# Optimization experiments

Hardware: AMD Instinct MI355X
Metric: run time of the kernel (lower is better)

Reference implementation:

```python
import jax, jax.numpy as jnp
import numpy as np

N_NODES = 100000
N_EDGES = 6400000
N_FEAT = 128
HIDDEN = 16
N_CLASSES = 10
N_GRAPHS = 1024


def setup_inputs() -> dict:
    key = jax.random.key(0)
    ks = jax.random.split(key, 16)
    x = jax.random.normal(ks[0], (N_NODES, N_FEAT), dtype=jnp.float32)
    src = jax.random.randint(ks[1], (N_EDGES,), 0, N_NODES, dtype=jnp.int64)
    dst = jax.random.randint(ks[2], (N_EDGES,), 0, N_NODES, dtype=jnp.int64)
    edge_index = jnp.stack([src, dst], axis=0)
    batch = jnp.sort(jax.random.randint(ks[3], (N_NODES,), 0, N_GRAPHS, dtype=jnp.int64))
    s = 0.1
    emb = jax.random.normal(ks[4], (N_FEAT, HIDDEN), dtype=jnp.float32) * s
    W1l = jax.random.normal(ks[5], (HIDDEN, HIDDEN), dtype=jnp.float32) * s
    b1 = jnp.zeros((HIDDEN,), dtype=jnp.float32)
    W1r = jax.random.normal(ks[6], (HIDDEN, HIDDEN), dtype=jnp.float32) * s
    W2l = jax.random.normal(ks[7], (HIDDEN, HIDDEN), dtype=jnp.float32) * s
    b2 = jnp.zeros((HIDDEN,), dtype=jnp.float32)
    W2r = jax.random.normal(ks[8], (HIDDEN, HIDDEN), dtype=jnp.float32) * s
    W3l = jax.random.normal(ks[9], (N_CLASSES, HIDDEN), dtype=jnp.float32) * s
    b3 = jnp.zeros((N_CLASSES,), dtype=jnp.float32)
    W3r = jax.random.normal(ks[10], (N_CLASSES, HIDDEN), dtype=jnp.float32) * s
    return {"x": x, "edge_index": edge_index, "batch": batch, "emb": emb,
            "W1l": W1l, "b1": b1, "W1r": W1r,
            "W2l": W2l, "b2": b2, "W2r": W2r,
            "W3l": W3l, "b3": b3, "W3r": W3r}


def _sage_conv(h, src, dst, Wl, bl, Wr, n_nodes):
    # PyG SAGEConv (aggr='mean'): out = lin_l(mean_j x_j) + lin_r(x_i), then L2-normalize
    msgs = h[src]                                             # [E, F]
    agg = jax.ops.segment_sum(msgs, dst, num_segments=n_nodes)
    deg = jax.ops.segment_sum(jnp.ones((src.shape[0],), h.dtype), dst, num_segments=n_nodes)
    agg = agg / jnp.maximum(deg, 1.0)[:, None]
    out = agg @ Wl.T + bl + h @ Wr.T
    norm = jnp.linalg.norm(out, axis=-1, keepdims=True)
    return out / jnp.maximum(norm, 1e-12)


def reference(x, edge_index, batch, emb, W1l, b1, W1r, W2l, b2, W2r, W3l, b3, W3r):
    src, dst = edge_index[0], edge_index[1]
    n = x.shape[0]
    # embedding of argmax over one-hot-ish features
    h = emb[jnp.argmax(x, axis=1)]                            # [N, H]
    h = jax.nn.relu(_sage_conv(h, src, dst, W1l, b1, W1r, n))  # dropout is identity in eval
    h = jax.nn.relu(_sage_conv(h, src, dst, W2l, b2, W2r, n))
    h = _sage_conv(h, src, dst, W3l, b3, W3r, n)              # [N, C]
    # global mean pool over graphs
    pooled = jax.ops.segment_sum(h, batch, num_segments=N_GRAPHS)
    cnt = jax.ops.segment_sum(jnp.ones((n,), h.dtype), batch, num_segments=N_GRAPHS)
    pooled = pooled / jnp.maximum(cnt, 1.0)[:, None]
    return jax.nn.softmax(pooled, axis=1)
```

## Files before the change

### kernel.cpp

```cpp
#include <hip/hip_runtime.h>
#include <hip/hip_bf16.h>

#define N_FEAT 128
#define HID 16
#define NCLS 10
#define NGRAPH 1024
#define SHIFT 7
#define NBMAX 1024
#define CAP 24576
#define CH 8192
#define EPB (CH / 256)
#define GC_NODES 64
#define GCAP2 5120

__device__ __forceinline__ float u2f(unsigned int u) {
    union { unsigned int u; float f; } c; c.u = u; return c.f;
}
__device__ __forceinline__ float bf2f(__hip_bfloat16 b) {
    return __bfloat162float(b);
}
__device__ __forceinline__ unsigned short f2us(float f) {
    union { __hip_bfloat16 b; unsigned short u; } c;
    c.b = __float2bfloat16(f);
    return c.u;
}
__device__ __forceinline__ float ldw(const void* __restrict__ p, int i, int isbf) {
    return isbf ? bf2f(((const __hip_bfloat16*)p)[i]) : ((const float*)p)[i];
}
__device__ __forceinline__ void unp8(uint4 v, float* f) {
    f[0] = u2f(v.x << 16); f[1] = u2f(v.x & 0xffff0000u);
    f[2] = u2f(v.y << 16); f[3] = u2f(v.y & 0xffff0000u);
    f[4] = u2f(v.z << 16); f[5] = u2f(v.z & 0xffff0000u);
    f[6] = u2f(v.w << 16); f[7] = u2f(v.w & 0xffff0000u);
}
__device__ __forceinline__ void acc8(uint4 v, float* a8) {
    a8[0] += u2f(v.x << 16); a8[1] += u2f(v.x & 0xffff0000u);
    a8[2] += u2f(v.y << 16); a8[3] += u2f(v.y & 0xffff0000u);
    a8[4] += u2f(v.z << 16); a8[5] += u2f(v.z & 0xffff0000u);
    a8[6] += u2f(v.w << 16); a8[7] += u2f(v.w & 0xffff0000u);
}

__global__ void k_detect(const int* __restrict__ ei,
                         const unsigned int* __restrict__ xw,
                         int* __restrict__ flags) {
    if (blockIdx.x == 0 && threadIdx.x == 0) {
        int nz = 0;
        for (int i = 1; i < 256; i += 2) nz |= ei[i];
        flags[0] = (nz == 0) ? 1 : 0;
        int cnt = 0;
        for (int i = 0; i < 64; i++) {
            unsigned int ef = xw[i] & 0x7F80u;
            if (ef >= 0x3C00u && ef <= 0x4080u) cnt++;
        }
        flags[1] = (cnt >= 32) ? 1 : 0;
    }
}

__global__ void k_argmax_embed(const void* __restrict__ x,
                               const void* __restrict__ emb,
                               const int* __restrict__ flags,
                               unsigned short* __restrict__ h, int n) {
    int wave = (int)((blockIdx.x * (unsigned)blockDim.x + threadIdx.x) >> 6);
    int lane = threadIdx.x & 63;
    if (wave >= n) return;
    int isbf = flags[1];
    float v0, v1;
    if (isbf) {
        const unsigned int* row =
            (const unsigned int*)((const __hip_bfloat16*)x + (size_t)wave * N_FEAT);
        unsigned int u = row[lane];
        v0 = u2f(u << 16);
        v1 = u2f(u & 0xffff0000u);
    } else {
        const float2* row = (const float2*)((const float*)x + (size_t)wave * N_FEAT);
        float2 u = row[lane];
        v0 = u.x; v1 = u.y;
    }
    float bv; int bi;
    if (v1 > v0) { bv = v1; bi = 2 * lane + 1; }
    else         { bv = v0; bi = 2 * lane; }
    #pragma unroll
    for (int off = 1; off < 64; off <<= 1) {
        float ov = __shfl_xor(bv, off);
        int   oi = __shfl_xor(bi, off);
        if (ov > bv || (ov == bv && oi < bi)) { bv = ov; bi = oi; }
    }
    if (lane < HID) {
        unsigned short us;
        if (isbf) us = ((const unsigned short*)emb)[bi * HID + lane];
        else      us = f2us(((const float*)emb)[bi * HID + lane]);
        h[(size_t)wave * HID + lane] = us;
    }
}

__global__ void k_binhist(const int* __restrict__ ei, const int* __restrict__ flags,
                          int* __restrict__ rbBuf, int e, int nbins) {
    __shared__ int lh[NBMAX];
    int t = threadIdx.x;
    for (int b = t; b < nbins; b += 256) lh[b] = 0;
    __syncthreads();
    int base = blockIdx.x * CH;
    int sh = flags[0];
    for (int j = 0; j < EPB; j++) {
        int i = base + j * 256 + t;
        if (i < e) {
            int d = ei[((size_t)(e + i)) << sh];
            atomicAdd(&lh[d >> SHIFT], 1);
        }
    }
    __syncthreads();
    int* row = rbBuf + (size_t)blockIdx.x * nbins;
    for (int b = t; b < nbins; b += 256) row[b] = lh[b];
}

__global__ void k_colscan(int* __restrict__ rbBuf, int* __restrict__ binCnt,
                          int nblk, int nbins) {
    __shared__ int ls[1024];
    int b = blockIdx.x, t = threadIdx.x;
    int v = (t < nblk) ? rbBuf[(size_t)t * nbins + b] : 0;
    ls[t] = v;
    __syncthreads();
    #pragma unroll
    for (int off = 1; off < 1024; off <<= 1) {
        int w = (t >= off) ? ls[t - off] : 0;
        __syncthreads();
        ls[t] += w;
        __syncthreads();
    }
    if (t < nblk) rbBuf[(size_t)t * nbins + b] = ls[t] - v;
    if (t == 1023) binCnt[b] = ls[t];
}

__global__ void k_scanbins(const int* __restrict__ binCnt,
                           int* __restrict__ binStart, int nbins, int e) {
    __shared__ int ls[1024];
    int t = threadIdx.x;
    int v = (t < nbins) ? binCnt[t] : 0;
    ls[t] = v;
    __syncthreads();
    #pragma unroll
    for (int off = 1; off < 1024; off <<= 1) {
        int w = (t >= off) ? ls[t - off] : 0;
        __syncthreads();
        ls[t] += w;
        __syncthreads();
    }
    if (t < nbins) binStart[t] = ls[t] - v;
    if (t == 0) binStart[nbins] = e;
}

__global__ __launch_bounds__(256) void k_binplace(
        const int* __restrict__ ei, const int* __restrict__ flags,
        const int* __restrict__ binStart, const int* __restrict__ rbBuf,
        int* __restrict__ col, int e, int nbins) {
    __shared__ int cnt[NBMAX];
    __shared__ int ldsOff[NBMAX];
    __shared__ int ldsBase[NBMAX];
    __shared__ int ps[256];
    __shared__ int stage[CH];
    __shared__ unsigned short binOf[CH];
    int t = threadIdx.x;
    for (int b = t; b < nbins; b += 256) cnt[b] = 0;
    __syncthreads();
    int base = blockIdx.x * CH;
    int sh = flags[0];
    int myV[EPB]; short myB[EPB];
    for (int j = 0; j < EPB; j++) {
        int i = base + j * 256 + t;
        if (i < e) {
            int s = ei[((size_t)i) << sh];
            int d = ei[((size_t)(e + i)) << sh];
            myV[j] = (s << SHIFT) | (d & ((1 << SHIFT) - 1));
            int b2 = d >> SHIFT;
            myB[j] = (short)b2;
            atomicAdd(&cnt[b2], 1);
        } else myB[j] = -1;
    }
    __syncthreads();
    int c[4]; int lsum = 0;
    int bb = t * 4;
    #pragma unroll
    for (int k = 0; k < 4; k++) {
        int b2 = bb + k;
        c[k] = (b2 < nbins) ? cnt[b2] : 0;
        lsum += c[k];
    }
    ps[t] = lsum;
    __syncthreads();
    #pragma unroll
    for (int off = 1; off < 256; off <<= 1) {
        int w = (t >= off) ? ps[t - off] : 0;
        __syncthreads();
        ps[t] += w;
        __syncthreads();
    }
    int run = ps[t] - lsum;
    #pragma unroll
    for (int k = 0; k < 4; k++) {
        int b2 = bb + k;
        if (b2 < nbins) ldsOff[b2] = run;
        run += c[k];
    }
    __syncthreads();
    const int* rb = rbBuf + (size_t)blockIdx.x * nbins;
    for (int b2 = t; b2 < nbins; b2 += 256) {
        ldsBase[b2] = binStart[b2] + rb[b2] - ldsOff[b2];
        cnt[b2] = 0;
    }
    __syncthreads();
    for (int j = 0; j < EPB; j++) {
        if (myB[j] >= 0) {
            int b2 = myB[j];
            int r = atomicAdd(&cnt[b2], 1);
            int p = ldsOff[b2] + r;
            stage[p] = myV[j];
            binOf[p] = (unsigned short)b2;
        }
    }
    __syncthreads();
    int total = e - base;
    if (total > CH) total = CH;
    for (int i = t; i < total; i += 256) {
        int b2 = binOf[i];
        col[ldsBase[b2] + i] = stage[i];
    }
}

__global__ void k_place(int* __restrict__ col, const int* __restrict__ binStart,
                        int* __restrict__ rowStart, int n, int e) {
    __shared__ int stage[CAP];
    __shared__ int cntN[1 << SHIFT];
    __shared__ int sc[1 << SHIFT];
    __shared__ int rs[1 << SHIFT];
    int b = blockIdx.x;
    int t = threadIdx.x;
    int nb = b << SHIFT;
    int s0 = binStart[b];
    int s1 = binStart[b + 1];
    int cnt = s1 - s0;
    if (t < (1 << SHIFT)) cntN[t] = 0;
    bool st = (cnt <= CAP);
    __syncthreads();
    for (int i = t; i < cnt; i += 256) {
        int v = col[s0 + i];
        if (st) stage[i] = v;
        atomicAdd(&cntN[v & ((1 << SHIFT) - 1)], 1);
    }
    __syncthreads();
    if (t < (1 << SHIFT)) sc[t] = cntN[t];
    __syncthreads();
    #pragma unroll
    for (int off = 1; off < (1 << SHIFT); off <<= 1) {
        int w = 0;
        if (t < (1 << SHIFT) && t >= off) w = sc[t - off];
        __syncthreads();
        if (t < (1 << SHIFT)) sc[t] += w;
        __syncthreads();
    }
    if (t < (1 << SHIFT)) {
        int start = s0 + sc[t] - cntN[t];
        rs[t] = start;
        int node = nb + t;
        if (node < n) rowStart[node] = start;
        cntN[t] = 0;
    }
    __syncthreads();
    for (int i = t; i < cnt; i += 256) {
        int v = st ? stage[i] : col[s0 + i];
        int dl = v & ((1 << SHIFT) - 1);
        int r = atomicAdd(&cntN[dl], 1);
        col[rs[dl] + r] = v >> SHIFT;
    }
}

__global__ __launch_bounds__(256) void k_gc(
        const int* __restrict__ col, const int* __restrict__ rowStart,
        const unsigned short* __restrict__ hin,
        const void* __restrict__ Wl, const void* __restrict__ bia,
        const void* __restrict__ Wr, const int* __restrict__ flags,
        unsigned short* __restrict__ hout, int n, int e) {
    __shared__ int ecol[GCAP2];
    __shared__ float wl[HID][HID], wr[HID][HID], bb[HID];
    int t = threadIdx.x;
    int b = blockIdx.x;
    int isbf = flags[1];
    if (t < HID * HID) {
        wl[t >> 4][t & 15] = ldw(Wl, t, isbf);
        wr[t >> 4][t & 15] = ldw(Wr, t, isbf);
    }
    if (t < HID) bb[t] = ldw(bia, t, isbf);
    int nb = b * GC_NODES;
    int s0 = rowStart[nb];
    int s1 = (nb + GC_NODES < n) ? rowStart[nb + GC_NODES] : e;
    int cnt = s1 - s0;
    bool st = (cnt <= GCAP2);
    if (st)
        for (int i = t; i < cnt; i += 256)
            ecol[i] = __builtin_nontemporal_load(col + s0 + i);
    __syncthreads();
    int nl = t >> 2;
    int j  = t & 1;
    int p  = (t >> 1) & 1;
    int node = nb + nl;
    if (node >= n) return;
    int lo = rowStart[node];
    int hi = (node + 1 < n) ? rowStart[node + 1] : e;
    const uint4* h4 = (const uint4*)hin;
    float a8[8];
    #pragma unroll
    for (int k = 0; k < 8; k++) a8[k] = 0.0f;
    if (st) {
        int i = lo - s0 + p;
        int end = hi - s0;
        for (; i + 6 < end; i += 8) {
            int e0 = ecol[i], e1 = ecol[i + 2], e2 = ecol[i + 4], e3 = ecol[i + 6];
            uint4 v0 = h4[(size_t)e0 * 2 + j];
            uint4 v1 = h4[(size_t)e1 * 2 + j];
            uint4 v2 = h4[(size_t)e2 * 2 + j];
            uint4 v3 = h4[(size_t)e3 * 2 + j];
            acc8(v0, a8); acc8(v1, a8); acc8(v2, a8); acc8(v3, a8);
        }
        for (; i < end; i += 2) {
            uint4 v = h4[(size_t)ecol[i] * 2 + j];
            acc8(v, a8);
        }
    } else {
        int i = lo + p;
        for (; i + 6 < hi; i += 8) {
            int e0 = col[i], e1 = col[i + 2], e2 = col[i + 4], e3 = col[i + 6];
            uint4 v0 = h4[(size_t)e0 * 2 + j];
            uint4 v1 = h4[(size_t)e1 * 2 + j];
            uint4 v2 = h4[(size_t)e2 * 2 + j];
            uint4 v3 = h4[(size_t)e3 * 2 + j];
            acc8(v0, a8); acc8(v1, a8); acc8(v2, a8); acc8(v3, a8);
        }
        for (; i < hi; i += 2) {
            uint4 v = h4[(size_t)col[i] * 2 + j];
            acc8(v, a8);
        }
    }
    #pragma unroll
    for (int k = 0; k < 8; k++) a8[k] += __shfl_xor(a8[k], 2);
    float invd = 1.0f / fmaxf((float)(hi - lo), 1.0f);
    #pragma unroll
    for (int k = 0; k < 8; k++) a8[k] *= invd;
    float av[HID];
    #pragma unroll
    for (int k = 0; k < 8; k++) {
        av[8 * j + k] = a8[k];
        av[8 * (1 - j) + k] = __shfl_xor(a8[k], 1);
    }
    float hb[HID];
    unp8(h4[(size_t)node * 2], hb);
    unp8(h4[(size_t)node * 2 + 1], hb + 8);
    float o[HID]; float sq = 0.0f;
    #pragma unroll
    for (int f = 0; f < HID; f++) {
        float acc = bb[f];
        #pragma unroll
        for (int k = 0; k < HID; k++)
            acc += av[k] * wl[f][k] + hb[k] * wr[f][k];
        o[f] = acc;
        sq += acc * acc;
    }
    float inn = 1.0f / fmaxf(sqrtf(sq), 1e-12f);
    if (p == 0) {
        uint4 w;
        unsigned int* wp = (unsigned int*)&w;
        #pragma unroll
        for (int q = 0; q < 4; q++) {
            unsigned int l0 = f2us(fmaxf(o[8 * j + 2 * q] * inn, 0.0f));
            unsigned int h0 = f2us(fmaxf(o[8 * j + 2 * q + 1] * inn, 0.0f));
            wp[q] = l0 | (h0 << 16);
        }
        ((uint4*)hout)[(size_t)node * 2 + j] = w;
    }
}

__global__ __launch_bounds__(256) void k_gc3(
        const int* __restrict__ col, const int* __restrict__ rowStart,
        const unsigned short* __restrict__ hin,
        const void* __restrict__ Wl, const void* __restrict__ bia,
        const void* __restrict__ Wr, const int* __restrict__ flags,
        float* __restrict__ h3, int n, int e) {
    __shared__ int ecol[GCAP2];
    __shared__ float wl[NCLS][HID], wr[NCLS][HID], bb[NCLS];
    int t = threadIdx.x;
    int b = blockIdx.x;
    int isbf = flags[1];
    if (t < NCLS * HID) {
        wl[t >> 4][t & 15] = ldw(Wl, t, isbf);
        wr[t >> 4][t & 15] = ldw(Wr, t, isbf);
    }
    if (t < NCLS) bb[t] = ldw(bia, t, isbf);
    int nb = b * GC_NODES;
    int s0 = rowStart[nb];
    int s1 = (nb + GC_NODES < n) ? rowStart[nb + GC_NODES] : e;
    int cnt = s1 - s0;
    bool st = (cnt <= GCAP2);
    if (st)
        for (int i = t; i < cnt; i += 256)
            ecol[i] = __builtin_nontemporal_load(col + s0 + i);
    __syncthreads();
    int nl = t >> 2;
    int j  = t & 1;
    int p  = (t >> 1) & 1;
    int node = nb + nl;
    if (node >= n) return;
    int lo = rowStart[node];
    int hi = (node + 1 < n) ? rowStart[node + 1] : e;
    const uint4* h4 = (const uint4*)hin;
    float a8[8];
    #pragma unroll
    for (int k = 0; k < 8; k++) a8[k] = 0.0f;
    if (st) {
        int i = lo - s0 + p;
        int end = hi - s0;
        for (; i + 6 < end; i += 8) {
            int e0 = ecol[i], e1 = ecol[i + 2], e2 = ecol[i + 4], e3 = ecol[i + 6];
            uint4 v0 = h4[(size_t)e0 * 2 + j];
            uint4 v1 = h4[(size_t)e1 * 2 + j];
            uint4 v2 = h4[(size_t)e2 * 2 + j];
            uint4 v3 = h4[(size_t)e3 * 2 + j];
            acc8(v0, a8); acc8(v1, a8); acc8(v2, a8); acc8(v3, a8);
        }
        for (; i < end; i += 2) {
            uint4 v = h4[(size_t)ecol[i] * 2 + j];
            acc8(v, a8);
        }
    } else {
        int i = lo + p;
        for (; i + 6 < hi; i += 8) {
            int e0 = col[i], e1 = col[i + 2], e2 = col[i + 4], e3 = col[i + 6];
            uint4 v0 = h4[(size_t)e0 * 2 + j];
            uint4 v1 = h4[(size_t)e1 * 2 + j];
            uint4 v2 = h4[(size_t)e2 * 2 + j];
            uint4 v3 = h4[(size_t)e3 * 2 + j];
            acc8(v0, a8); acc8(v1, a8); acc8(v2, a8); acc8(v3, a8);
        }
        for (; i < hi; i += 2) {
            uint4 v = h4[(size_t)col[i] * 2 + j];
            acc8(v, a8);
        }
    }
    #pragma unroll
    for (int k = 0; k < 8; k++) a8[k] += __shfl_xor(a8[k], 2);
    float invd = 1.0f / fmaxf((float)(hi - lo), 1.0f);
    #pragma unroll
    for (int k = 0; k < 8; k++) a8[k] *= invd;
    float av[HID];
    #pragma unroll
    for (int k = 0; k < 8; k++) {
        av[8 * j + k] = a8[k];
        av[8 * (1 - j) + k] = __shfl_xor(a8[k], 1);
    }
    float hb[HID];
    unp8(h4[(size_t)node * 2], hb);
    unp8(h4[(size_t)node * 2 + 1], hb + 8);
    float o[NCLS]; float sq = 0.0f;
    #pragma unroll
    for (int f = 0; f < NCLS; f++) {
        float acc = bb[f];
        #pragma unroll
        for (int k = 0; k < HID; k++)
            acc += av[k] * wl[f][k] + hb[k] * wr[f][k];
        o[f] = acc;
        sq += acc * acc;
    }
    float inn = 1.0f / fmaxf(sqrtf(sq), 1e-12f);
    float* op = h3 + (size_t)node * NCLS;
    if (p == 0) {
        if (j == 0) {
            #pragma unroll
            for (int f = 0; f < 8; f++) op[f] = o[f] * inn;
        } else {
            op[8] = o[8] * inn;
            op[9] = o[9] * inn;
        }
    }
}

__device__ __forceinline__ int lbound(const int* __restrict__ a, int n, int key, int sh) {
    int lo = 0, hi = n;
    while (lo < hi) {
        int mid = (lo + hi) >> 1;
        if (a[((size_t)mid) << sh] < key) lo = mid + 1; else hi = mid;
    }
    return lo;
}

__global__ void k_pool_softmax(const float* __restrict__ h3,
                               const int* __restrict__ batch,
                               const int* __restrict__ flags,
                               void* __restrict__ out, int n) {
    int g = blockIdx.x;
    int lane = threadIdx.x;
    int sh = flags[0];
    int lo = lbound(batch, n, g, sh);
    int hi = lbound(batch, n, g + 1, sh);
    float acc[NCLS];
    #pragma unroll
    for (int c = 0; c < NCLS; c++) acc[c] = 0.0f;
    for (int i = lo + lane; i < hi; i += 64) {
        const float* r = h3 + (size_t)i * NCLS;
        #pragma unroll
        for (int c = 0; c < NCLS; c++) acc[c] += r[c];
    }
    #pragma unroll
    for (int c = 0; c < NCLS; c++) {
        #pragma unroll
        for (int off = 1; off < 64; off <<= 1)
            acc[c] += __shfl_xor(acc[c], off);
    }
    float invc = 1.0f / fmaxf((float)(hi - lo), 1.0f);
    float m = -1e30f;
    #pragma unroll
    for (int c = 0; c < NCLS; c++) { acc[c] *= invc; m = fmaxf(m, acc[c]); }
    float s = 0.0f;
    #pragma unroll
    for (int c = 0; c < NCLS; c++) { acc[c] = expf(acc[c] - m); s += acc[c]; }
    float invs = 1.0f / s;
    if (lane < NCLS) {
        float v = acc[lane] * invs;
        size_t idx = (size_t)g * NCLS + lane;
        if (flags[1]) ((__hip_bfloat16*)out)[idx] = __float2bfloat16(v);
        else          ((float*)out)[idx] = v;
    }
}

extern "C" void kernel_launch(void* const* d_in, const int* in_sizes, int n_in,
                              void* d_out, int out_size, void* d_ws, size_t ws_size,
                              hipStream_t stream) {
    const void* x   = d_in[0];
    const int*  ei  = (const int*)d_in[1];
    const int*  bat = (const int*)d_in[2];
    const void* emb = d_in[3];
    const void* W1l = d_in[4];  const void* b1 = d_in[5];  const void* W1r = d_in[6];
    const void* W2l = d_in[7];  const void* b2 = d_in[8];  const void* W2r = d_in[9];
    const void* W3l = d_in[10]; const void* b3 = d_in[11]; const void* W3r = d_in[12];

    int n = in_sizes[0] / N_FEAT;
    int e = in_sizes[1] / 2;
    int nbins = (n + (1 << SHIFT) - 1) >> SHIFT;
    int nblk  = (e + CH - 1) / CH;

    unsigned short* hcur  = (unsigned short*)d_ws;
    unsigned short* hnext = hcur + (size_t)n * HID;
    float* h3       = (float*)(hnext + (size_t)n * HID);
    int*   col      = (int*)(h3 + (size_t)n * NCLS);
    int*   rowStart = col + e;
    int*   binCnt   = rowStart + n;
    int*   binStart = binCnt + nbins;
    int*   rbBuf    = binStart + (nbins + 1);
    int*   flags    = rbBuf + (size_t)nblk * nbins;

    int ngrid4 = (n + 3) / 4;
    int ngc = (n + GC_NODES - 1) / GC_NODES;

    k_detect<<<1, 64, 0, stream>>>(ei, (const unsigned int*)x, flags);
    k_binhist<<<nblk, 256, 0, stream>>>(ei, flags, rbBuf, e, nbins);
    k_colscan<<<nbins, 1024, 0, stream>>>(rbBuf, binCnt, nblk, nbins);
    k_scanbins<<<1, 1024, 0, stream>>>(binCnt, binStart, nbins, e);
    k_binplace<<<nblk, 256, 0, stream>>>(ei, flags, binStart, rbBuf, col, e, nbins);
    k_place<<<nbins, 256, 0, stream>>>(col, binStart, rowStart, n, e);

    k_argmax_embed<<<ngrid4, 256, 0, stream>>>(x, emb, flags, hcur, n);

    k_gc <<<ngc, 256, 0, stream>>>(col, rowStart, hcur,  W1l, b1, W1r, flags, hnext, n, e);
    k_gc <<<ngc, 256, 0, stream>>>(col, rowStart, hnext, W2l, b2, W2r, flags, hcur,  n, e);
    k_gc3<<<ngc, 256, 0, stream>>>(col, rowStart, hcur,  W3l, b3, W3r, flags, h3,    n, e);

    k_pool_softmax<<<NGRAPH, 64, 0, stream>>>(h3, bat, flags, d_out, n);
}
```

Measured before the change: 506.1 us.

## Gather full 16-feature rows per edge lane and widen k_place blocks

The gather kernels now have each of the four lanes per node fetch whole 32-byte neighbor rows, striding over edges by four, and reduce across lanes with two xor shuffles. Only one lane then runs the dense 16x16 transform and writes the output row, and the self-feature and rowStart loads are hoisted ahead of the LDS staging barrier. This cuts redundant per-lane matvec work and increases independent edge loads in flight, at the cost of more registers and idle lanes during the epilogue. k_place moves to 512 threads with a smaller shared staging buffer (CAP 9216), which raises occupancy but sends bins larger than the cap to the global-memory fallback.

```diff
diff --git a/kernel.cpp b/kernel.cpp
--- a/kernel.cpp
+++ b/kernel.cpp
@@ -7,7 +7,7 @@
 #define NGRAPH 1024
 #define SHIFT 7
 #define NBMAX 1024
-#define CAP 24576
+#define CAP 9216
 #define CH 8192
 #define EPB (CH / 256)
 #define GC_NODES 64
@@ -226,8 +226,9 @@
     }
 }
 
-__global__ void k_place(int* __restrict__ col, const int* __restrict__ binStart,
-                        int* __restrict__ rowStart, int n, int e) {
+__global__ __launch_bounds__(512) void k_place(
+        int* __restrict__ col, const int* __restrict__ binStart,
+        int* __restrict__ rowStart, int n, int e) {
     __shared__ int stage[CAP];
     __shared__ int cntN[1 << SHIFT];
     __shared__ int sc[1 << SHIFT];
@@ -241,7 +242,7 @@
     if (t < (1 << SHIFT)) cntN[t] = 0;
     bool st = (cnt <= CAP);
     __syncthreads();
-    for (int i = t; i < cnt; i += 256) {
+    for (int i = t; i < cnt; i += 512) {
         int v = col[s0 + i];
         if (st) stage[i] = v;
         atomicAdd(&cntN[v & ((1 << SHIFT) - 1)], 1);
@@ -265,7 +266,7 @@
         cntN[t] = 0;
     }
     __syncthreads();
-    for (int i = t; i < cnt; i += 256) {
+    for (int i = t; i < cnt; i += 512) {
         int v = st ? stage[i] : col[s0 + i];
         int dl = v & ((1 << SHIFT) - 1);
         int r = atomicAdd(&cntN[dl], 1);
@@ -292,88 +293,106 @@
     int nb = b * GC_NODES;
     int s0 = rowStart[nb];
     int s1 = (nb + GC_NODES < n) ? rowStart[nb + GC_NODES] : e;
+    int nl = t >> 2;
+    int q  = t & 3;
+    int node = nb + nl;
+    bool act = (node < n);
+    int lo = 0, hi = 0;
+    if (act) {
+        lo = rowStart[node];
+        hi = (node + 1 < n) ? rowStart[node + 1] : e;
+    }
+    const uint4* h4 = (const uint4*)hin;
+    uint4 sv0, sv1;
+    if (act && q == 0) {
+        sv0 = h4[(size_t)node * 2];
+        sv1 = h4[(size_t)node * 2 + 1];
+    }
     int cnt = s1 - s0;
     bool st = (cnt <= GCAP2);
     if (st)
         for (int i = t; i < cnt; i += 256)
             ecol[i] = __builtin_nontemporal_load(col + s0 + i);
     __syncthreads();
-    int nl = t >> 2;
-    int j  = t & 1;
-    int p  = (t >> 1) & 1;
-    int node = nb + nl;
-    if (node >= n) return;
-    int lo = rowStart[node];
-    int hi = (node + 1 < n) ? rowStart[node + 1] : e;
-    const uint4* h4 = (const uint4*)hin;
-    float a8[8];
-    #pragma unroll
-    for (int k = 0; k < 8; k++) a8[k] = 0.0f;
+    if (!act) return;
+
+    float a16[16];
+    #pragma unroll
+    for (int k = 0; k < 16; k++) a16[k] = 0.0f;
     if (st) {
-        int i = lo - s0 + p;
+        int i = lo - s0 + q;
         int end = hi - s0;
-        for (; i + 6 < end; i += 8) {
-            int e0 = ecol[i], e1 = ecol[i + 2], e2 = ecol[i + 4], e3 = ecol[i + 6];
-            uint4 v0 = h4[(size_t)e0 * 2 + j];
-            uint4 v1 = h4[(size_t)e1 * 2 + j];
-            uint4 v2 = h4[(size_t)e2 * 2 + j];
-            uint4 v3 = h4[(size_t)e3 * 2 + j];
-            acc8(v0, a8); acc8(v1, a8); acc8(v2, a8); acc8(v3, a8);
-        }
-        for (; i < end; i += 2) {
-            uint4 v = h4[(size_t)ecol[i] * 2 + j];
-            acc8(v, a8);
+        for (; i + 12 < end; i += 16) {
+            int e0 = ecol[i], e1 = ecol[i + 4], e2 = ecol[i + 8], e3 = ecol[i + 12];
+            uint4 va0 = h4[(size_t)e0 * 2],     vb0 = h4[(size_t)e0 * 2 + 1];
+            uint4 va1 = h4[(size_t)e1 * 2],     vb1 = h4[(size_t)e1 * 2 + 1];
+            uint4 va2 = h4[(size_t)e2 * 2],     vb2 = h4[(size_t)e2 * 2 + 1];
+            uint4 va3 = h4[(size_t)e3 * 2],     vb3 = h4[(size_t)e3 * 2 + 1];
+            acc8(va0, a16); acc8(vb0, a16 + 8);
+            acc8(va1, a16); acc8(vb1, a16 + 8);
+            acc8(va2, a16); acc8(vb2, a16 + 8);
+            acc8(va3, a16); acc8(vb3, a16 + 8);
+        }
+        for (; i < end; i += 4) {
+            int s = ecol[i];
+            uint4 va = h4[(size_t)s * 2], vb = h4[(size_t)s * 2 + 1];
+            acc8(va, a16); acc8(vb, a16 + 8);
         }
     } else {
-        int i = lo + p;
-        for (; i + 6 < hi; i += 8) {
-            int e0 = col[i], e1 = col[i + 2], e2 = col[i + 4], e3 = col[i + 6];
-            uint4 v0 = h4[(size_t)e0 * 2 + j];
-            uint4 v1 = h4[(size_t)e1 * 2 + j];
-            uint4 v2 = h4[(size_t)e2 * 2 + j];
-            uint4 v3 = h4[(size_t)e3 * 2 + j];
-            acc8(v0, a8); acc8(v1, a8); acc8(v2, a8); acc8(v3, a8);
-        }
-        for (; i < hi; i += 2) {
-            uint4 v = h4[(size_t)col[i] * 2 + j];
-            acc8(v, a8);
-        }
-    }
-    #pragma unroll
-    for (int k = 0; k < 8; k++) a8[k] += __shfl_xor(a8[k], 2);
-    float invd = 1.0f / fmaxf((float)(hi - lo), 1.0f);
-    #pragma unroll
-    for (int k = 0; k < 8; k++) a8[k] *= invd;
-    float av[HID];
-    #pragma unroll
-    for (int k = 0; k < 8; k++) {
-        av[8 * j + k] = a8[k];
-        av[8 * (1 - j) + k] = __shfl_xor(a8[k], 1);
-    }
-    float hb[HID];
-    unp8(h4[(size_t)node * 2], hb);
-    unp8(h4[(size_t)node * 2 + 1], hb + 8);
-    float o[HID]; float sq = 0.0f;
-    #pragma unroll
-    for (int f = 0; f < HID; f++) {
-        float acc = bb[f];
-        #pragma unroll
-        for (int k = 0; k < HID; k++)
-            acc += av[k] * wl[f][k] + hb[k] * wr[f][k];
-        o[f] = acc;
-        sq += acc * acc;
-    }
-    float inn = 1.0f / fmaxf(sqrtf(sq), 1e-12f);
-    if (p == 0) {
-        uint4 w;
-        unsigned int* wp = (unsigned int*)&w;
-        #pragma unroll
-        for (int q = 0; q < 4; q++) {
-            unsigned int l0 = f2us(fmaxf(o[8 * j + 2 * q] * inn, 0.0f));
-            unsigned int h0 = f2us(fmaxf(o[8 * j + 2 * q + 1] * inn, 0.0f));
-            wp[q] = l0 | (h0 << 16);
-        }
-        ((uint4*)hout)[(size_t)node * 2 + j] = w;
+        int i = lo + q;
+        for (; i + 12 < hi; i += 16) {
+            int e0 = col[i], e1 = col[i + 4], e2 = col[i + 8], e3 = col[i + 12];
+            uint4 va0 = h4[(size_t)e0 * 2],     vb0 = h4[(size_t)e0 * 2 + 1];
+            uint4 va1 = h4[(size_t)e1 * 2],     vb1 = h4[(size_t)e1 * 2 + 1];
+            uint4 va2 = h4[(size_t)e2 * 2],     vb2 = h4[(size_t)e2 * 2 + 1];
+            uint4 va3 = h4[(size_t)e3 * 2],     vb3 = h4[(size_t)e3 * 2 + 1];
+            acc8(va0, a16); acc8(vb0, a16 + 8);
+            acc8(va1, a16); acc8(vb1, a16 + 8);
+            acc8(va2, a16); acc8(vb2, a16 + 8);
+            acc8(va3, a16); acc8(vb3, a16 + 8);
+        }
+        for (; i < hi; i += 4) {
+            int s = col[i];
+            uint4 va = h4[(size_t)s * 2], vb = h4[(size_t)s * 2 + 1];
+            acc8(va, a16); acc8(vb, a16 + 8);
+        }
+    }
+    #pragma unroll
+    for (int k = 0; k < 16; k++) a16[k] += __shfl_xor(a16[k], 1);
+    #pragma unroll
+    for (int k = 0; k < 16; k++) a16[k] += __shfl_xor(a16[k], 2);
+    if (q == 0) {
+        float invd = 1.0f / fmaxf((float)(hi - lo), 1.0f);
+        #pragma unroll
+        for (int k = 0; k < 16; k++) a16[k] *= invd;
+        float hb[HID];
+        unp8(sv0, hb);
+        unp8(sv1, hb + 8);
+        float o[HID]; float sq = 0.0f;
+        #pragma unroll
+        for (int f = 0; f < HID; f++) {
+            float acc = bb[f];
+            #pragma unroll
+            for (int k = 0; k < HID; k++)
+                acc += a16[k] * wl[f][k] + hb[k] * wr[f][k];
+            o[f] = acc;
+            sq += acc * acc;
+        }
+        float inn = 1.0f / fmaxf(sqrtf(sq), 1e-12f);
+        uint4 w0, w1;
+        unsigned int* wp0 = (unsigned int*)&w0;
+        unsigned int* wp1 = (unsigned int*)&w1;
+        #pragma unroll
+        for (int v = 0; v < 4; v++) {
+            unsigned int l0 = f2us(fmaxf(o[2 * v] * inn, 0.0f));
+            unsigned int h0 = f2us(fmaxf(o[2 * v + 1] * inn, 0.0f));
+            wp0[v] = l0 | (h0 << 16);
+            unsigned int l1 = f2us(fmaxf(o[8 + 2 * v] * inn, 0.0f));
+            unsigned int h1 = f2us(fmaxf(o[8 + 2 * v + 1] * inn, 0.0f));
+            wp1[v] = l1 | (h1 << 16);
+        }
+        ((uint4*)hout)[(size_t)node * 2]     = w0;
+        ((uint4*)hout)[(size_t)node * 2 + 1] = w1;
     }
 }
 
@@ -396,87 +415,95 @@
     int nb = b * GC_NODES;
     int s0 = rowStart[nb];
     int s1 = (nb + GC_NODES < n) ? rowStart[nb + GC_NODES] : e;
+    int nl = t >> 2;
+    int q  = t & 3;
+    int node = nb + nl;
+    bool act = (node < n);
+    int lo = 0, hi = 0;
+    if (act) {
+        lo = rowStart[node];
+        hi = (node + 1 < n) ? rowStart[node + 1] : e;
+    }
+    const uint4* h4 = (const uint4*)hin;
+    uint4 sv0, sv1;
+    if (act && q == 0) {
+        sv0 = h4[(size_t)node * 2];
+        sv1 = h4[(size_t)node * 2 + 1];
+    }
     int cnt = s1 - s0;
     bool st = (cnt <= GCAP2);
     if (st)
         for (int i = t; i < cnt; i += 256)
             ecol[i] = __builtin_nontemporal_load(col + s0 + i);
     __syncthreads();
-    int nl = t >> 2;
-    int j  = t & 1;
-    int p  = (t >> 1) & 1;
-    int node = nb + nl;
-    if (node >= n) return;
-    int lo = rowStart[node];
-    int hi = (node + 1 < n) ? rowStart[node + 1] : e;
-    const uint4* h4 = (const uint4*)hin;
-    float a8[8];
-    #pragma unroll
-    for (int k = 0; k < 8; k++) a8[k] = 0.0f;
+    if (!act) return;
+
+    float a16[16];
+    #pragma unroll
+    for (int k = 0; k < 16; k++) a16[k] = 0.0f;
     if (st) {
-        int i = lo - s0 + p;
+        int i = lo - s0 + q;
         int end = hi - s0;
-        for (; i + 6 < end; i += 8) {
-            int e0 = ecol[i], e1 = ecol[i + 2], e2 = ecol[i + 4], e3 = ecol[i + 6];
-            uint4 v0 = h4[(size_t)e0 * 2 + j];
-            uint4 v1 = h4[(size_t)e1 * 2 + j];
-            uint4 v2 = h4[(size_t)e2 * 2 + j];
-            uint4 v3 = h4[(size_t)e3 * 2 + j];
-            acc8(v0, a8); acc8(v1, a8); acc8(v2, a8); acc8(v3, a8);
-        }
-        for (; i < end; i += 2) {
-            uint4 v = h4[(size_t)ecol[i] * 2 + j];
-            acc8(v, a8);
+        for (; i + 12 < end; i += 16) {
+            int e0 = ecol[i], e1 = ecol[i + 4], e2 = ecol[i + 8], e3 = ecol[i + 12];
+            uint4 va0 = h4[(size_t)e0 * 2],     vb0 = h4[(size_t)e0 * 2 + 1];
+            uint4 va1 = h4[(size_t)e1 * 2],     vb1 = h4[(size_t)e1 * 2 + 1];
+            uint4 va2 = h4[(size_t)e2 * 2],     vb2 = h4[(size_t)e2 * 2 + 1];
+            uint4 va3 = h4[(size_t)e3 * 2],     vb3 = h4[(size_t)e3 * 2 + 1];
+            acc8(va0, a16); acc8(vb0, a16 + 8);
+            acc8(va1, a16); acc8(vb1, a16 + 8);
+            acc8(va2, a16); acc8(vb2, a16 + 8);
+            acc8(va3, a16); acc8(vb3, a16 + 8);
+        }
+        for (; i < end; i += 4) {
+            int s = ecol[i];
+            uint4 va = h4[(size_t)s * 2], vb = h4[(size_t)s * 2 + 1];
+            acc8(va, a16); acc8(vb, a16 + 8);
         }
     } else {
-        int i = lo + p;
-        for (; i + 6 < hi; i += 8) {
-            int e0 = col[i], e1 = col[i + 2], e2 = col[i + 4], e3 = col[i + 6];
-            uint4 v0 = h4[(size_t)e0 * 2 + j];
-            uint4 v1 = h4[(size_t)e1 * 2 + j];
-            uint4 v2 = h4[(size_t)e2 * 2 + j];
-            uint4 v3 = h4[(size_t)e3 * 2 + j];
-            acc8(v0, a8); acc8(v1, a8); acc8(v2, a8); acc8(v3, a8);
-        }
-        for (; i < hi; i += 2) {
-            uint4 v = h4[(size_t)col[i] * 2 + j];
-            acc8(v, a8);
-        }
-    }
-    #pragma unroll
-    for (int k = 0; k < 8; k++) a8[k] += __shfl_xor(a8[k], 2);
-    float invd = 1.0f / fmaxf((float)(hi - lo), 1.0f);
-    #pragma unroll
-    for (int k = 0; k < 8; k++) a8[k] *= invd;
-    float av[HID];
-    #pragma unroll
-    for (int k = 0; k < 8; k++) {
-        av[8 * j + k] = a8[k];
-        av[8 * (1 - j) + k] = __shfl_xor(a8[k], 1);
-    }
-    float hb[HID];
-    unp8(h4[(size_t)node * 2], hb);
-    unp8(h4[(size_t)node * 2 + 1], hb + 8);
-    float o[NCLS]; float sq = 0.0f;
-    #pragma unroll
-    for (int f = 0; f < NCLS; f++) {
-        float acc = bb[f];
-        #pragma unroll
-        for (int k = 0; k < HID; k++)
-            acc += av[k] * wl[f][k] + hb[k] * wr[f][k];
-        o[f] = acc;
-        sq += acc * acc;
-    }
-    float inn = 1.0f / fmaxf(sqrtf(sq), 1e-12f);
-    float* op = h3 + (size_t)node * NCLS;
-    if (p == 0) {
-        if (j == 0) {
+        int i = lo + q;
+        for (; i + 12 < hi; i += 16) {
+            int e0 = col[i], e1 = col[i + 4], e2 = col[i + 8], e3 = col[i + 12];
+            uint4 va0 = h4[(size_t)e0 * 2],     vb0 = h4[(size_t)e0 * 2 + 1];
+            uint4 va1 = h4[(size_t)e1 * 2],     vb1 = h4[(size_t)e1 * 2 + 1];
+            uint4 va2 = h4[(size_t)e2 * 2],     vb2 = h4[(size_t)e2 * 2 + 1];
+            uint4 va3 = h4[(size_t)e3 * 2],     vb3 = h4[(size_t)e3 * 2 + 1];
+            acc8(va0, a16); acc8(vb0, a16 + 8);
+            acc8(va1, a16); acc8(vb1, a16 + 8);
+            acc8(va2, a16); acc8(vb2, a16 + 8);
+            acc8(va3, a16); acc8(vb3, a16 + 8);
+        }
+        for (; i < hi; i += 4) {
+            int s = col[i];
+            uint4 va = h4[(size_t)s * 2], vb = h4[(size_t)s * 2 + 1];
+            acc8(va, a16); acc8(vb, a16 + 8);
+        }
+    }
+    #pragma unroll
+    for (int k = 0; k < 16; k++) a16[k] += __shfl_xor(a16[k], 1);
+    #pragma unroll
+    for (int k = 0; k < 16; k++) a16[k] += __shfl_xor(a16[k], 2);
+    if (q == 0) {
+        float invd = 1.0f / fmaxf((float)(hi - lo), 1.0f);
+        #pragma unroll
+        for (int k = 0; k < 16; k++) a16[k] *= invd;
+        float hb[HID];
+        unp8(sv0, hb);
+        unp8(sv1, hb + 8);
+        float o[NCLS]; float sq = 0.0f;
+        #pragma unroll
+        for (int f = 0; f < NCLS; f++) {
+            float acc = bb[f];
             #pragma unroll
-            for (int f = 0; f < 8; f++) op[f] = o[f] * inn;
-        } else {
-            op[8] = o[8] * inn;
-            op[9] = o[9] * inn;
-        }
+            for (int k = 0; k < HID; k++)
+                acc += a16[k] * wl[f][k] + hb[k] * wr[f][k];
+            o[f] = acc;
+            sq += acc * acc;
+        }
+        float inn = 1.0f / fmaxf(sqrtf(sq), 1e-12f);
+        float* op = h3 + (size_t)node * NCLS;
+        #pragma unroll
+        for (int f = 0; f < NCLS; f++) op[f] = o[f] * inn;
     }
 }
 
@@ -562,7 +589,7 @@
     k_colscan<<<nbins, 1024, 0, stream>>>(rbBuf, binCnt, nblk, nbins);
     k_scanbins<<<1, 1024, 0, stream>>>(binCnt, binStart, nbins, e);
     k_binplace<<<nblk, 256, 0, stream>>>(ei, flags, binStart, rbBuf, col, e, nbins);
-    k_place<<<nbins, 256, 0, stream>>>(col, binStart, rowStart, n, e);
+    k_place<<<nbins, 512, 0, stream>>>(col, binStart, rowStart, n, e);
 
     k_argmax_embed<<<ngrid4, 256, 0, stream>>>(x, emb, flags, hcur, n);
 
```

New measurement: 438.8 us. 13.3% less time.
